# Performance work log

Measured on AMD Instinct MI355X. Metric: run time of the kernel, lower is better.

The kernel has to match this reference:

```python
import jax, jax.numpy as jnp
import numpy as np

B, N, KD, VD = 2048, 131072, 256, 256

def setup_inputs() -> dict:
    key = jax.random.key(0)
    k1, k2, k3 = jax.random.split(key, 3)
    query = jax.random.normal(k1, (B, KD), dtype=jnp.float32)
    keys = jax.random.normal(k2, (N, KD), dtype=jnp.float32)
    vals = jax.random.normal(k3, (N, VD), dtype=jnp.float32)
    return {"query": query, "keys": keys, "vals": vals, "top_k": 8}

def reference(query, keys, vals, top_k):
    # Pairwise L2 distance via the matmul identity (same math as
    # torch.norm(q[:,None]-k[None], dim=-1), avoids B x N x D intermediate):
    # ||q - k||^2 = ||q||^2 + ||k||^2 - 2 q.k
    q2 = jnp.sum(query * query, axis=-1, keepdims=True)          # [B, 1]
    k2 = jnp.sum(keys * keys, axis=-1)                           # [N]
    qk = jnp.einsum('bd,nd->bn', query, keys)                    # [B, N]
    dist = jnp.sqrt(jnp.maximum(q2 + k2[None, :] - 2.0 * qk, 0.0))
    # top-k smallest distances -> negate and take top-k largest
    _, indices = jax.lax.top_k(-dist, top_k)                     # [B, k]
    retrieved = vals[indices]                                    # [B, k, VD]
    return retrieved
```

## Files before the change

kernel.cpp:

```cpp
#include <hip/hip_runtime.h>
#include <hip/hip_bf16.h>
#include <cstdint>

#define B_Q    2048
#define N_K    131072
#define KD     256
#define VD     256
#define TOPK   8

#define TK     32
#define NCHUNK 64
#define CHUNK  (N_K / NCHUNK)
#define CTILES (CHUNK / TK)
#define QB     256
#define QTILES (B_Q / QB)
#define QBS    256
#define NBUF   4
#define TILE_B (TK * KD * 2)
#define SSTEPS 8
#define SLOTS  32
#define OVCAP  8192
#define NSUB   16
#define TAU_MARGIN 2.0f
#define SENTF  0x7F800000u

typedef short bf16x8 __attribute__((ext_vector_type(8)));
typedef float f32x4  __attribute__((ext_vector_type(4)));

__device__ __forceinline__ unsigned short f2bf(float x) {
    uint32_t u = __float_as_uint(x);
    uint32_t r = (u + 0x7FFFu + ((u >> 16) & 1u)) >> 16;
    return (unsigned short)r;
}

__device__ __forceinline__ bool lex_lt(float d1, int i1, float d2, int i2) {
    return (d1 < d2) || (d1 == d2 && i1 < i2);
}

__device__ __forceinline__ uint32_t umin32(uint32_t a, uint32_t b) { return a < b ? a : b; }
__device__ __forceinline__ uint32_t umax32(uint32_t a, uint32_t b) { return a > b ? a : b; }
__device__ __forceinline__ unsigned long long umin64(unsigned long long a, unsigned long long b) { return a < b ? a : b; }

__device__ __forceinline__ void gld16(const void* g, void* l) {
    __builtin_amdgcn_global_load_lds(
        (const __attribute__((address_space(1))) unsigned int*)g,
        (__attribute__((address_space(3))) unsigned int*)l, 16, 0, 0);
}
__device__ __forceinline__ void gld4(const void* g, void* l) {
    __builtin_amdgcn_global_load_lds(
        (const __attribute__((address_space(1))) unsigned int*)g,
        (__attribute__((address_space(3))) unsigned int*)l, 4, 0, 0);
}

__device__ __forceinline__ void ins8u(uint32_t v, uint32_t (&c)[8]) {
    if (v < c[7]) {
        c[7] = v;
        #pragma unroll
        for (int p = 7; p > 0; --p)
            if (c[p] < c[p - 1]) { uint32_t t = c[p]; c[p] = c[p - 1]; c[p - 1] = t; }
    }
}

__global__ void qprep_kernel(const float* __restrict__ q, float* __restrict__ q2,
                             unsigned short* __restrict__ qa) {
    int gw   = (blockIdx.x * blockDim.x + threadIdx.x) >> 6;
    int lane = threadIdx.x & 63;
    float4 v = reinterpret_cast<const float4*>(q + (size_t)gw * KD)[lane];
    float s = v.x * v.x + v.y * v.y + v.z * v.z + v.w * v.w;
    #pragma unroll
    for (int off = 32; off > 0; off >>= 1) s += __shfl_down(s, off, 64);
    if (lane == 0) q2[gw] = s;
    ushort4 u;
    u.x = f2bf(-2.f * v.x); u.y = f2bf(-2.f * v.y);
    u.z = f2bf(-2.f * v.z); u.w = f2bf(-2.f * v.w);
    *reinterpret_cast<ushort4*>(qa + (size_t)gw * KD + lane * 4) = u;
}

__global__ __launch_bounds__(256) void kperm2_kernel(
    const float* __restrict__ keys, unsigned short* __restrict__ kp,
    float* __restrict__ k2) {
    __shared__ float psum[32][33];
    const int gt = blockIdx.x, tid = threadIdx.x;
    #pragma unroll
    for (int u = 0; u < 4; ++u) {
        int unit = u * 256 + tid;
        int row  = unit >> 5;
        int grp  = unit & 31;
        const float* src = keys + (size_t)(gt * 32 + row) * KD + grp * 8;
        float4 a = *reinterpret_cast<const float4*>(src);
        float4 b = *reinterpret_cast<const float4*>(src + 4);
        psum[row][grp] = a.x * a.x + a.y * a.y + a.z * a.z + a.w * a.w
                       + b.x * b.x + b.y * b.y + b.z * b.z + b.w * b.w;
        uint4 pack;
        pack.x = (uint32_t)f2bf(a.x) | ((uint32_t)f2bf(a.y) << 16);
        pack.y = (uint32_t)f2bf(a.z) | ((uint32_t)f2bf(a.w) << 16);
        pack.z = (uint32_t)f2bf(b.x) | ((uint32_t)f2bf(b.y) << 16);
        pack.w = (uint32_t)f2bf(b.z) | ((uint32_t)f2bf(b.w) << 16);
        int s  = grp >> 2;
        int ki = row >> 4;
        int l  = ((grp & 3) << 4) | (row & 15);
        size_t o = ((((size_t)gt * 8 + s) * 2 + ki) * 64 + l);
        *reinterpret_cast<uint4*>(kp + o * 8) = pack;
    }
    __syncthreads();
    if (tid < 32) {
        float s = 0.f;
        #pragma unroll
        for (int g = 0; g < 32; ++g) s += psum[tid][g];
        k2[gt * 32 + tid] = s;
    }
}

__global__ __launch_bounds__(512, 2) void sample_kernel(
    const unsigned short* __restrict__ qaug, const char* __restrict__ kperm,
    const float* __restrict__ k2, uint32_t* __restrict__ subtop) {

    __shared__ __align__(16) char  lds[TILE_B];
    __shared__ __align__(16) float k2l[64];

    const int tid = threadIdx.x;
    const int w   = tid >> 6;
    const int l   = tid & 63;
    const int l15 = l & 15;
    const int l4  = l >> 4;
    const int sub = blockIdx.x & (NSUB - 1);
    const int qt  = blockIdx.x >> 4;
    const int q0  = qt * QBS;

    bf16x8 af[2][SSTEPS];
    #pragma unroll
    for (int qf = 0; qf < 2; ++qf)
        #pragma unroll
        for (int s = 0; s < SSTEPS; ++s) {
            int qr = q0 + w * 32 + qf * 16 + l15;
            af[qf][s] = *reinterpret_cast<const bf16x8*>(
                qaug + (size_t)qr * KD + s * 32 + l4 * 8);
        }

    uint32_t cnd[2][4][8];
    #pragma unroll
    for (int qf = 0; qf < 2; ++qf)
        #pragma unroll
        for (int j = 0; j < 4; ++j)
            #pragma unroll
            for (int s = 0; s < 8; ++s) cnd[qf][j][s] = SENTF;

    for (int i = 0; i < 4; ++i) {
        int t = sub * 4 + i;
        __syncthreads();
        const char* src = kperm + (size_t)t * TILE_B;
        #pragma unroll
        for (int i2 = 0; i2 < 2; ++i2) {
            int seg = w * 2 + i2;
            gld16(src + seg * 1024 + l * 16, &lds[seg * 1024]);
        }
        gld4(k2 + t * TK + l, &k2l[0]);
        __syncthreads();

        float k2v[2];
        #pragma unroll
        for (int ki = 0; ki < 2; ++ki) k2v[ki] = k2l[ki * 16 + l15] + 256.0f;

        f32x4 acc[2][2];
        #pragma unroll
        for (int qf = 0; qf < 2; ++qf)
            #pragma unroll
            for (int ki = 0; ki < 2; ++ki) acc[qf][ki] = (f32x4){0.f, 0.f, 0.f, 0.f};

        #pragma unroll
        for (int s = 0; s < SSTEPS; ++s) {
            bf16x8 bfr[2];
            #pragma unroll
            for (int ki = 0; ki < 2; ++ki)
                bfr[ki] = *reinterpret_cast<const bf16x8*>(&lds[((s * 2 + ki) * 64 + l) * 16]);
            #pragma unroll
            for (int ki = 0; ki < 2; ++ki) {
                acc[0][ki] = __builtin_amdgcn_mfma_f32_16x16x32_bf16(af[0][s], bfr[ki], acc[0][ki], 0, 0, 0);
                acc[1][ki] = __builtin_amdgcn_mfma_f32_16x16x32_bf16(af[1][s], bfr[ki], acc[1][ki], 0, 0, 0);
            }
        }

        #pragma unroll
        for (int qf = 0; qf < 2; ++qf)
            #pragma unroll
            for (int j = 0; j < 4; ++j) {
                ins8u(__float_as_uint(k2v[0] + acc[qf][0][j]), cnd[qf][j]);
                ins8u(__float_as_uint(k2v[1] + acc[qf][1][j]), cnd[qf][j]);
            }
    }

    #pragma unroll
    for (int qf = 0; qf < 2; ++qf)
        #pragma unroll
        for (int j = 0; j < 4; ++j) {
            uint32_t c[8];
            #pragma unroll
            for (int s = 0; s < 8; ++s) c[s] = cnd[qf][j][s];
            #pragma unroll
            for (int mask = 1; mask <= 8; mask <<= 1) {
                uint32_t o[8], m[8];
                #pragma unroll
                for (int s = 0; s < 8; ++s)
                    o[s] = (uint32_t)__shfl_xor((int)c[s], mask, 64);
                #pragma unroll
                for (int s = 0; s < 8; ++s) m[s] = umin32(c[s], o[7 - s]);
                #define CX(a,b) { uint32_t lo = umin32(m[a], m[b]); uint32_t hi = umax32(m[a], m[b]); m[a] = lo; m[b] = hi; }
                CX(0,4) CX(1,5) CX(2,6) CX(3,7)
                CX(0,2) CX(1,3) CX(4,6) CX(5,7)
                CX(0,1) CX(2,3) CX(4,5) CX(6,7)
                #undef CX
                #pragma unroll
                for (int s = 0; s < 8; ++s) c[s] = m[s];
            }
            if (l15 == 0) {
                int q = q0 + w * 32 + qf * 16 + l4 * 4 + j;
                uint32_t* dst = subtop + ((size_t)q * NSUB + sub) * 8;
                uint4 a = {c[0], c[1], c[2], c[3]};
                uint4 b = {c[4], c[5], c[6], c[7]};
                *reinterpret_cast<uint4*>(dst)     = a;
                *reinterpret_cast<uint4*>(dst + 4) = b;
            }
        }
}

__global__ __launch_bounds__(256) void tau_kernel(
    const uint32_t* __restrict__ subtop, float* __restrict__ taug,
    uint32_t* __restrict__ ovcnt) {
    const int tid = threadIdx.x, l = tid & 63;
    const int q = blockIdx.x * 4 + (tid >> 6);
    uint32_t a = subtop[(size_t)q * 128 + l];
    uint32_t b = subtop[(size_t)q * 128 + 64 + l];
    uint32_t c[8];
    c[0] = umin32(a, b); c[1] = umax32(a, b);
    #pragma unroll
    for (int s = 2; s < 8; ++s) c[s] = SENTF;
    #pragma unroll
    for (int mask = 1; mask <= 32; mask <<= 1) {
        uint32_t o[8], m[8];
        #pragma unroll
        for (int s = 0; s < 8; ++s)
            o[s] = (uint32_t)__shfl_xor((int)c[s], mask, 64);
        #pragma unroll
        for (int s = 0; s < 8; ++s) m[s] = umin32(c[s], o[7 - s]);
        #define CX(x,y) { uint32_t lo = umin32(m[x], m[y]); uint32_t hi = umax32(m[x], m[y]); m[x] = lo; m[y] = hi; }
        CX(0,4) CX(1,5) CX(2,6) CX(3,7)
        CX(0,2) CX(1,3) CX(4,6) CX(5,7)
        CX(0,1) CX(2,3) CX(4,5) CX(6,7)
        #undef CX
        #pragma unroll
        for (int s = 0; s < 8; ++s) c[s] = m[s];
    }
    if (l == 0) taug[q] = __uint_as_float(c[7]) + TAU_MARGIN;
    if (blockIdx.x == 0 && tid == 0) *ovcnt = 0;
}

__global__ __launch_bounds__(1024, 4) void phase1_kernel(
    const unsigned short* __restrict__ qaug, const char* __restrict__ kperm,
    const float* __restrict__ k2, const float* __restrict__ taug,
    uint32_t* __restrict__ list, uint32_t* __restrict__ cnt2,
    uint32_t* __restrict__ ovcnt, unsigned long long* __restrict__ ovlist) {

    __shared__ __align__(16) char     lds[NBUF][TILE_B];
    __shared__ __align__(16) float    k2l[NBUF][64];
    __shared__            uint32_t    scnt[QB];

    const int tid   = threadIdx.x;
    const int w     = tid >> 6;
    const int p     = w >> 1;
    const int ki    = w & 1;
    const int l     = tid & 63;
    const int l15   = l & 15;
    const int l4    = l >> 4;
    const int chunk = blockIdx.x & (NCHUNK - 1);
    const int qt    = blockIdx.x >> 6;
    const int q0    = qt * QB;
    const char*  kpb = kperm + (size_t)chunk * ((size_t)CTILES * TILE_B);
    const float* k2c = k2 + (size_t)chunk * CHUNK;

    if (tid < QB) scnt[tid] = 0;

    bf16x8 af[2][SSTEPS];
    float  tau[2][4];
    #pragma unroll
    for (int qf = 0; qf < 2; ++qf) {
        #pragma unroll
        for (int s = 0; s < SSTEPS; ++s) {
            int qr = q0 + p * 32 + qf * 16 + l15;
            af[qf][s] = *reinterpret_cast<const bf16x8*>(
                qaug + (size_t)qr * KD + s * 32 + l4 * 8);
        }
        #pragma unroll
        for (int j = 0; j < 4; ++j)
            tau[qf][j] = taug[q0 + p * 32 + qf * 16 + l4 * 4 + j];
    }

    auto STAGE = [&](int t) {
        int buf = t & (NBUF - 1);
        const char* src = kpb + (size_t)t * TILE_B;
        gld16(src + w * 1024 + l * 16, &lds[buf][w * 1024]);
        gld4(k2c + t * TK + l, &k2l[buf][0]);
    };

    STAGE(0); STAGE(1); STAGE(2);

    for (int t = 0; t < CTILES; ++t) {
        const int buf = t & (NBUF - 1);
        if (t < CTILES - 2)       asm volatile("s_waitcnt vmcnt(4)" ::: "memory");
        else if (t == CTILES - 2) asm volatile("s_waitcnt vmcnt(2)" ::: "memory");
        else                      asm volatile("s_waitcnt vmcnt(0)" ::: "memory");
        __builtin_amdgcn_s_barrier();
        __builtin_amdgcn_sched_barrier(0);

        const char* lb = &lds[buf][0];
        const float k2v = k2l[buf][ki * 16 + l15] + 256.0f;

        f32x4 acc[2];
        acc[0] = (f32x4){0.f, 0.f, 0.f, 0.f};
        acc[1] = (f32x4){0.f, 0.f, 0.f, 0.f};

        #pragma unroll
        for (int s = 0; s < SSTEPS; ++s) {
            bf16x8 bfr = *reinterpret_cast<const bf16x8*>(lb + ((s * 2 + ki) * 64 + l) * 16);
            acc[0] = __builtin_amdgcn_mfma_f32_16x16x32_bf16(af[0][s], bfr, acc[0], 0, 0, 0);
            acc[1] = __builtin_amdgcn_mfma_f32_16x16x32_bf16(af[1][s], bfr, acc[1], 0, 0, 0);
        }

        const uint32_t kb = (uint32_t)(t * TK + ki * 16 + l15);
        #pragma unroll
        for (int qf = 0; qf < 2; ++qf)
            #pragma unroll
            for (int j = 0; j < 4; ++j) {
                float v0 = k2v + acc[qf][j];
                if (v0 < tau[qf][j]) {
                    int ql = p * 32 + qf * 16 + l4 * 4 + j;
                    uint32_t slot = atomicAdd(&scnt[ql], 1u);
                    uint32_t e = (__float_as_uint(v0) & 0xFFFFF800u) | kb;
                    if (slot < SLOTS) {
                        list[(((size_t)(q0 + ql) * NCHUNK + chunk) << 5) + slot] = e;
                    } else {
                        uint32_t op = atomicAdd(ovcnt, 1u);
                        if (op < OVCAP)
                            ovlist[op] = ((unsigned long long)__float_as_uint(v0) << 32)
                                       | ((unsigned long long)(uint32_t)(q0 + ql) << 17)
                                       | (uint32_t)(chunk * CHUNK + kb);
                    }
                }
            }

        if (t + 3 < CTILES) STAGE(t + 3);
    }

    __syncthreads();
    if (tid < QB) cnt2[(size_t)(q0 + tid) * NCHUNK + chunk] = umin32(scnt[tid], SLOTS);
}

__global__ __launch_bounds__(256) void phase2_kernel(
    const uint32_t* __restrict__ list, const uint32_t* __restrict__ cnt2,
    const uint32_t* __restrict__ ovcnt, const unsigned long long* __restrict__ ovlist,
    const float* __restrict__ query, const float* __restrict__ keys,
    const float* __restrict__ q2g, const float* __restrict__ k2g,
    const float* __restrict__ vals, float* __restrict__ out) {

    __shared__ uint32_t cc[NCHUNK];
    __shared__ unsigned long long ovq[64];
    __shared__ uint32_t nov;
    __shared__ int topg[64];
    __shared__ float td2[64];
    __shared__ int fin[8];

    const int q = blockIdx.x, tid = threadIdx.x, w = tid >> 6, l = tid & 63;

    if (tid < NCHUNK) cc[tid] = cnt2[(size_t)q * NCHUNK + tid];
    if (tid < 64) ovq[tid] = ~0ull;
    if (tid == 0) nov = 0;
    __syncthreads();
    uint32_t on = umin32(*ovcnt, OVCAP);
    for (uint32_t i = tid; i < on; i += 256) {
        unsigned long long e = ovlist[i];
        if (((e >> 17) & 0x7FFull) == (unsigned long long)q) {
            uint32_t p = atomicAdd(&nov, 1u);
            if (p < 64)
                ovq[p] = ((unsigned long long)((uint32_t)(e >> 32) >> 11) << 17)
                       | (uint32_t)(e & 0x1FFFFull);
        }
    }
    __syncthreads();

    unsigned long long v[9];
    #pragma unroll
    for (int j = 0; j < 9; ++j) {
        int idx = j * 64 + l;
        unsigned long long key = ~0ull;
        if (idx < 512) {
            int c = w * 16 + (idx >> 5), s = idx & 31;
            if ((uint32_t)s < cc[c]) {
                uint32_t e = list[(((size_t)q * NCHUNK + c) << 5) + s];
                key = ((unsigned long long)(e >> 11) << 17)
                    | (uint32_t)(c * CHUNK + (e & 0x7FFu));
            }
        } else if (idx < 528) {
            key = ovq[w * 16 + (idx - 512)];
        }
        v[j] = key;
    }

    for (int r = 0; r < 16; ++r) {
        unsigned long long bv = v[0];
        #pragma unroll
        for (int j = 1; j < 9; ++j) bv = umin64(bv, v[j]);
        #pragma unroll
        for (int off = 32; off > 0; off >>= 1) {
            unsigned long long ov = __shfl_xor(bv, off, 64);
            bv = umin64(bv, ov);
        }
        if (l == 0) topg[w * 16 + r] = (bv == ~0ull) ? -1 : (int)(uint32_t)(bv & 0x1FFFFull);
        #pragma unroll
        for (int j = 0; j < 9; ++j) if (v[j] == bv) v[j] = ~0ull;
    }
    __syncthreads();

    float4 qv = reinterpret_cast<const float4*>(query + (size_t)q * KD)[l];
    for (int r = w; r < 64; r += 4) {
        int gk = topg[r];
        if (gk >= 0) {
            float4 kv = reinterpret_cast<const float4*>(keys + (size_t)gk * KD)[l];
            float d = qv.x * kv.x + qv.y * kv.y + qv.z * kv.z + qv.w * kv.w;
            #pragma unroll
            for (int off = 32; off > 0; off >>= 1) d += __shfl_down(d, off, 64);
            if (l == 0) td2[r] = fmaxf(q2g[q] + k2g[gk] - 2.0f * d, 0.0f);
        } else if (l == 0) {
            td2[r] = INFINITY;
        }
    }
    __syncthreads();

    if (tid == 0) {
        float fd[8]; int fi[8];
        #pragma unroll
        for (int s = 0; s < 8; ++s) { fd[s] = INFINITY; fi[s] = 0x7fffffff; }
        for (int i = 0; i < 64; ++i) {
            if (topg[i] < 0) continue;
            float d2 = td2[i]; int gk = topg[i];
            if (lex_lt(d2, gk, fd[7], fi[7])) {
                fd[7] = d2; fi[7] = gk;
                #pragma unroll
                for (int p = 7; p > 0; --p)
                    if (lex_lt(fd[p], fi[p], fd[p - 1], fi[p - 1])) {
                        float t1 = fd[p]; fd[p] = fd[p - 1]; fd[p - 1] = t1;
                        int   t2 = fi[p]; fi[p] = fi[p - 1]; fi[p - 1] = t2;
                    }
            }
        }
        #pragma unroll
        for (int s = 0; s < 8; ++s) fin[s] = fi[s];
    }
    __syncthreads();

    for (int r = w; r < TOPK; r += 4) {
        float4 v2 = reinterpret_cast<const float4*>(vals + (size_t)fin[r] * VD)[l];
        reinterpret_cast<float4*>(out + ((size_t)q * TOPK + r) * VD)[l] = v2;
    }
}

extern "C" void kernel_launch(void* const* d_in, const int* in_sizes, int n_in,
                              void* d_out, int out_size, void* d_ws, size_t ws_size,
                              hipStream_t stream) {
    const float* query = (const float*)d_in[0];
    const float* keys  = (const float*)d_in[1];
    const float* vals  = (const float*)d_in[2];
    float* out = (float*)d_out;

    char* ws = (char*)d_ws;
    float*              q2     = (float*)(ws);
    float*              k2     = (float*)(ws + 8192);
    unsigned short*     qaug   = (unsigned short*)(ws + 533504);
    unsigned short*     kperm  = (unsigned short*)(ws + 1582080);
    uint32_t*           list   = (uint32_t*)(ws + 68690944);
    uint32_t*           subtop = (uint32_t*)(ws + 68690944);
    uint32_t*           cnt2   = (uint32_t*)(ws + 85468160);
    float*              taug   = (float*)(ws + 85992448);
    uint32_t*           ovcnt  = (uint32_t*)(ws + 86000640);
    unsigned long long* ovlist = (unsigned long long*)(ws + 86004736);

    qprep_kernel<<<B_Q / 4, 256, 0, stream>>>(query, q2, qaug);
    kperm2_kernel<<<N_K / 32, 256, 0, stream>>>(keys, kperm, k2);
    sample_kernel<<<(B_Q / QBS) * NSUB, 512, 0, stream>>>(qaug, (const char*)kperm, k2, subtop);
    tau_kernel<<<B_Q / 4, 256, 0, stream>>>(subtop, taug, ovcnt);
    phase1_kernel<<<NCHUNK * QTILES, 1024, 0, stream>>>(qaug, (const char*)kperm, k2,
                                                        taug, list, cnt2, ovcnt, ovlist);
    phase2_kernel<<<B_Q, 256, 0, stream>>>(list, cnt2, ovcnt, ovlist,
                                           query, keys, q2, k2, vals, out);
}
```

Baseline: 300.9 us.

## Switch phase1 to 32x32x16 MFMA with new key permutation layout

Phase1 now uses the 32x32x16 bf16 MFMA, with each wave computing a full 32-query by 32-key tile. Blocks shrink to 512 threads, and each thread stages two segments per tile. The key-permute kernel writes a new layout that matches the 32x32 B-fragment. Because that layout no longer fits the 16x16 sample kernel, the sample kernel now reads fp32 keys directly and converts them to bf16 into LDS itself. The larger MFMA shape is meant to cut LDS fragment reads and instruction count per FLOP, at the cost of more accumulator registers and fewer waves per block.

```diff
diff --git a/kernel.cpp b/kernel.cpp
--- a/kernel.cpp
+++ b/kernel.cpp
@@ -18,6 +18,7 @@
 #define NBUF   4
 #define TILE_B (TK * KD * 2)
 #define SSTEPS 8
+#define KSTEPS 16
 #define SLOTS  32
 #define OVCAP  8192
 #define NSUB   16
@@ -26,6 +27,7 @@
 
 typedef short bf16x8 __attribute__((ext_vector_type(8)));
 typedef float f32x4  __attribute__((ext_vector_type(4)));
+typedef float f32x16 __attribute__((ext_vector_type(16)));
 
 __device__ __forceinline__ unsigned short f2bf(float x) {
     uint32_t u = __float_as_uint(x);
@@ -96,10 +98,10 @@
         pack.y = (uint32_t)f2bf(a.z) | ((uint32_t)f2bf(a.w) << 16);
         pack.z = (uint32_t)f2bf(b.x) | ((uint32_t)f2bf(b.y) << 16);
         pack.w = (uint32_t)f2bf(b.z) | ((uint32_t)f2bf(b.w) << 16);
-        int s  = grp >> 2;
-        int ki = row >> 4;
-        int l  = ((grp & 3) << 4) | (row & 15);
-        size_t o = ((((size_t)gt * 8 + s) * 2 + ki) * 64 + l);
+        int kk   = grp >> 1;
+        int g    = grp & 1;
+        int lane = g * 32 + row;
+        size_t o = (((size_t)gt * KSTEPS + kk) * 64 + lane);
         *reinterpret_cast<uint4*>(kp + o * 8) = pack;
     }
     __syncthreads();
@@ -112,11 +114,10 @@
 }
 
 __global__ __launch_bounds__(512, 2) void sample_kernel(
-    const unsigned short* __restrict__ qaug, const char* __restrict__ kperm,
+    const unsigned short* __restrict__ qaug, const float* __restrict__ keys,
     const float* __restrict__ k2, uint32_t* __restrict__ subtop) {
 
-    __shared__ __align__(16) char  lds[TILE_B];
-    __shared__ __align__(16) float k2l[64];
+    __shared__ __align__(16) char lds[TILE_B];
 
     const int tid = threadIdx.x;
     const int w   = tid >> 6;
@@ -148,18 +149,30 @@
     for (int i = 0; i < 4; ++i) {
         int t = sub * 4 + i;
         __syncthreads();
-        const char* src = kperm + (size_t)t * TILE_B;
-        #pragma unroll
-        for (int i2 = 0; i2 < 2; ++i2) {
-            int seg = w * 2 + i2;
-            gld16(src + seg * 1024 + l * 16, &lds[seg * 1024]);
-        }
-        gld4(k2 + t * TK + l, &k2l[0]);
+        #pragma unroll
+        for (int uu = 0; uu < 2; ++uu) {
+            int unit = uu * 512 + tid;
+            int row  = unit >> 5;
+            int grp  = unit & 31;
+            const float* src = keys + (size_t)(t * 32 + row) * KD + grp * 8;
+            float4 a = *reinterpret_cast<const float4*>(src);
+            float4 b = *reinterpret_cast<const float4*>(src + 4);
+            uint4 pack;
+            pack.x = (uint32_t)f2bf(a.x) | ((uint32_t)f2bf(a.y) << 16);
+            pack.y = (uint32_t)f2bf(a.z) | ((uint32_t)f2bf(a.w) << 16);
+            pack.z = (uint32_t)f2bf(b.x) | ((uint32_t)f2bf(b.y) << 16);
+            pack.w = (uint32_t)f2bf(b.z) | ((uint32_t)f2bf(b.w) << 16);
+            int s    = grp >> 2;
+            int g    = grp & 3;
+            int lane = g * 16 + (row & 15);
+            int ki   = row >> 4;
+            *reinterpret_cast<uint4*>(&lds[((s * 2 + ki) * 64 + lane) * 16]) = pack;
+        }
         __syncthreads();
 
         float k2v[2];
         #pragma unroll
-        for (int ki = 0; ki < 2; ++ki) k2v[ki] = k2l[ki * 16 + l15] + 256.0f;
+        for (int ki = 0; ki < 2; ++ki) k2v[ki] = k2[t * TK + ki * 16 + l15] + 256.0f;
 
         f32x4 acc[2][2];
         #pragma unroll
@@ -254,7 +267,7 @@
     if (blockIdx.x == 0 && tid == 0) *ovcnt = 0;
 }
 
-__global__ __launch_bounds__(1024, 4) void phase1_kernel(
+__global__ __launch_bounds__(512, 4) void phase1_kernel(
     const unsigned short* __restrict__ qaug, const char* __restrict__ kperm,
     const float* __restrict__ k2, const float* __restrict__ taug,
     uint32_t* __restrict__ list, uint32_t* __restrict__ cnt2,
@@ -266,11 +279,9 @@
 
     const int tid   = threadIdx.x;
     const int w     = tid >> 6;
-    const int p     = w >> 1;
-    const int ki    = w & 1;
     const int l     = tid & 63;
-    const int l15   = l & 15;
-    const int l4    = l >> 4;
+    const int l31   = l & 31;
+    const int lg    = l >> 5;
     const int chunk = blockIdx.x & (NCHUNK - 1);
     const int qt    = blockIdx.x >> 6;
     const int q0    = qt * QB;
@@ -279,25 +290,26 @@
 
     if (tid < QB) scnt[tid] = 0;
 
-    bf16x8 af[2][SSTEPS];
-    float  tau[2][4];
-    #pragma unroll
-    for (int qf = 0; qf < 2; ++qf) {
-        #pragma unroll
-        for (int s = 0; s < SSTEPS; ++s) {
-            int qr = q0 + p * 32 + qf * 16 + l15;
-            af[qf][s] = *reinterpret_cast<const bf16x8*>(
-                qaug + (size_t)qr * KD + s * 32 + l4 * 8);
-        }
-        #pragma unroll
-        for (int j = 0; j < 4; ++j)
-            tau[qf][j] = taug[q0 + p * 32 + qf * 16 + l4 * 4 + j];
-    }
+    bf16x8 af[KSTEPS];
+    const int qr = q0 + w * 32 + l31;
+    #pragma unroll
+    for (int kk = 0; kk < KSTEPS; ++kk)
+        af[kk] = *reinterpret_cast<const bf16x8*>(
+            qaug + (size_t)qr * KD + kk * 16 + lg * 8);
+
+    float tau[16];
+    #pragma unroll
+    for (int r = 0; r < 16; ++r)
+        tau[r] = taug[q0 + w * 32 + (r & 3) + 8 * (r >> 2) + 4 * lg];
 
     auto STAGE = [&](int t) {
         int buf = t & (NBUF - 1);
         const char* src = kpb + (size_t)t * TILE_B;
-        gld16(src + w * 1024 + l * 16, &lds[buf][w * 1024]);
+        #pragma unroll
+        for (int i = 0; i < 2; ++i) {
+            int seg = w * 2 + i;
+            gld16(src + seg * 1024 + l * 16, &lds[buf][seg * 1024]);
+        }
         gld4(k2c + t * TK + l, &k2l[buf][0]);
     };
 
@@ -305,47 +317,42 @@
 
     for (int t = 0; t < CTILES; ++t) {
         const int buf = t & (NBUF - 1);
-        if (t < CTILES - 2)       asm volatile("s_waitcnt vmcnt(4)" ::: "memory");
-        else if (t == CTILES - 2) asm volatile("s_waitcnt vmcnt(2)" ::: "memory");
+        if (t < CTILES - 2)       asm volatile("s_waitcnt vmcnt(6)" ::: "memory");
+        else if (t == CTILES - 2) asm volatile("s_waitcnt vmcnt(3)" ::: "memory");
         else                      asm volatile("s_waitcnt vmcnt(0)" ::: "memory");
         __builtin_amdgcn_s_barrier();
         __builtin_amdgcn_sched_barrier(0);
 
         const char* lb = &lds[buf][0];
-        const float k2v = k2l[buf][ki * 16 + l15] + 256.0f;
-
-        f32x4 acc[2];
-        acc[0] = (f32x4){0.f, 0.f, 0.f, 0.f};
-        acc[1] = (f32x4){0.f, 0.f, 0.f, 0.f};
-
-        #pragma unroll
-        for (int s = 0; s < SSTEPS; ++s) {
-            bf16x8 bfr = *reinterpret_cast<const bf16x8*>(lb + ((s * 2 + ki) * 64 + l) * 16);
-            acc[0] = __builtin_amdgcn_mfma_f32_16x16x32_bf16(af[0][s], bfr, acc[0], 0, 0, 0);
-            acc[1] = __builtin_amdgcn_mfma_f32_16x16x32_bf16(af[1][s], bfr, acc[1], 0, 0, 0);
-        }
-
-        const uint32_t kb = (uint32_t)(t * TK + ki * 16 + l15);
-        #pragma unroll
-        for (int qf = 0; qf < 2; ++qf)
-            #pragma unroll
-            for (int j = 0; j < 4; ++j) {
-                float v0 = k2v + acc[qf][j];
-                if (v0 < tau[qf][j]) {
-                    int ql = p * 32 + qf * 16 + l4 * 4 + j;
-                    uint32_t slot = atomicAdd(&scnt[ql], 1u);
-                    uint32_t e = (__float_as_uint(v0) & 0xFFFFF800u) | kb;
-                    if (slot < SLOTS) {
-                        list[(((size_t)(q0 + ql) * NCHUNK + chunk) << 5) + slot] = e;
-                    } else {
-                        uint32_t op = atomicAdd(ovcnt, 1u);
-                        if (op < OVCAP)
-                            ovlist[op] = ((unsigned long long)__float_as_uint(v0) << 32)
-                                       | ((unsigned long long)(uint32_t)(q0 + ql) << 17)
-                                       | (uint32_t)(chunk * CHUNK + kb);
-                    }
+        const float k2v = k2l[buf][l31] + 256.0f;
+
+        f32x16 acc = (f32x16){0.f, 0.f, 0.f, 0.f, 0.f, 0.f, 0.f, 0.f,
+                              0.f, 0.f, 0.f, 0.f, 0.f, 0.f, 0.f, 0.f};
+        #pragma unroll
+        for (int kk = 0; kk < KSTEPS; ++kk) {
+            bf16x8 bfr = *reinterpret_cast<const bf16x8*>(lb + ((kk * 64 + l) * 16));
+            acc = __builtin_amdgcn_mfma_f32_32x32x16_bf16(af[kk], bfr, acc, 0, 0, 0);
+        }
+
+        const uint32_t kb = (uint32_t)(t * TK + l31);
+        #pragma unroll
+        for (int r = 0; r < 16; ++r) {
+            float v0 = k2v + acc[r];
+            if (v0 < tau[r]) {
+                int ql = w * 32 + (r & 3) + 8 * (r >> 2) + 4 * lg;
+                uint32_t slot = atomicAdd(&scnt[ql], 1u);
+                uint32_t e = (__float_as_uint(v0) & 0xFFFFF800u) | kb;
+                if (slot < SLOTS) {
+                    list[(((size_t)(q0 + ql) * NCHUNK + chunk) << 5) + slot] = e;
+                } else {
+                    uint32_t op = atomicAdd(ovcnt, 1u);
+                    if (op < OVCAP)
+                        ovlist[op] = ((unsigned long long)__float_as_uint(v0) << 32)
+                                   | ((unsigned long long)(uint32_t)(q0 + ql) << 17)
+                                   | (uint32_t)(chunk * CHUNK + kb);
                 }
             }
+        }
 
         if (t + 3 < CTILES) STAGE(t + 3);
     }
@@ -484,10 +491,10 @@
 
     qprep_kernel<<<B_Q / 4, 256, 0, stream>>>(query, q2, qaug);
     kperm2_kernel<<<N_K / 32, 256, 0, stream>>>(keys, kperm, k2);
-    sample_kernel<<<(B_Q / QBS) * NSUB, 512, 0, stream>>>(qaug, (const char*)kperm, k2, subtop);
+    sample_kernel<<<(B_Q / QBS) * NSUB, 512, 0, stream>>>(qaug, keys, k2, subtop);
     tau_kernel<<<B_Q / 4, 256, 0, stream>>>(subtop, taug, ovcnt);
-    phase1_kernel<<<NCHUNK * QTILES, 1024, 0, stream>>>(qaug, (const char*)kperm, k2,
-                                                        taug, list, cnt2, ovcnt, ovlist);
+    phase1_kernel<<<NCHUNK * QTILES, 512, 0, stream>>>(qaug, (const char*)kperm, k2,
+                                                       taug, list, cnt2, ovcnt, ovlist);
     phase2_kernel<<<B_Q, 256, 0, stream>>>(list, cnt2, ovcnt, ovlist,
                                            query, keys, q2, k2, vals, out);
 }
```

Measured after the change: 340.9 us. +13.3%, slower.

## Shrink phase1 blocks to four waves each covering both key halves

Applied to the files above, without the earlier changes.

The phase1 distance-filter kernel drops from 1024-thread blocks over 256 queries to 256-thread blocks over 128 queries. Each wave now computes a 32-query by 32-key tile, reusing its query fragments across both 16-key halves. Each wave issues four LDS-staging loads per tile, and the vmcnt waits are adjusted to match. This aims to cut barrier cost across many waves and improve per-wave MFMA reuse. In exchange, each key tile is shared by half as many queries, so global key traffic doubles, the grid doubles, and per-thread register use rises.

```diff
diff --git a/kernel.cpp b/kernel.cpp
--- a/kernel.cpp
+++ b/kernel.cpp
@@ -12,7 +12,7 @@
 #define NCHUNK 64
 #define CHUNK  (N_K / NCHUNK)
 #define CTILES (CHUNK / TK)
-#define QB     256
+#define QB     128
 #define QTILES (B_Q / QB)
 #define QBS    256
 #define NBUF   4
@@ -254,7 +254,7 @@
     if (blockIdx.x == 0 && tid == 0) *ovcnt = 0;
 }
 
-__global__ __launch_bounds__(1024, 4) void phase1_kernel(
+__global__ __launch_bounds__(256, 2) void phase1_kernel(
     const unsigned short* __restrict__ qaug, const char* __restrict__ kperm,
     const float* __restrict__ k2, const float* __restrict__ taug,
     uint32_t* __restrict__ list, uint32_t* __restrict__ cnt2,
@@ -266,8 +266,6 @@
 
     const int tid   = threadIdx.x;
     const int w     = tid >> 6;
-    const int p     = w >> 1;
-    const int ki    = w & 1;
     const int l     = tid & 63;
     const int l15   = l & 15;
     const int l4    = l >> 4;
@@ -285,19 +283,23 @@
     for (int qf = 0; qf < 2; ++qf) {
         #pragma unroll
         for (int s = 0; s < SSTEPS; ++s) {
-            int qr = q0 + p * 32 + qf * 16 + l15;
+            int qr = q0 + w * 32 + qf * 16 + l15;
             af[qf][s] = *reinterpret_cast<const bf16x8*>(
                 qaug + (size_t)qr * KD + s * 32 + l4 * 8);
         }
         #pragma unroll
         for (int j = 0; j < 4; ++j)
-            tau[qf][j] = taug[q0 + p * 32 + qf * 16 + l4 * 4 + j];
+            tau[qf][j] = taug[q0 + w * 32 + qf * 16 + l4 * 4 + j];
     }
 
     auto STAGE = [&](int t) {
         int buf = t & (NBUF - 1);
         const char* src = kpb + (size_t)t * TILE_B;
-        gld16(src + w * 1024 + l * 16, &lds[buf][w * 1024]);
+        #pragma unroll
+        for (int i = 0; i < 4; ++i) {
+            int seg = w * 4 + i;
+            gld16(src + seg * 1024 + l * 16, &lds[buf][seg * 1024]);
+        }
         gld4(k2c + t * TK + l, &k2l[buf][0]);
     };
 
@@ -305,47 +307,59 @@
 
     for (int t = 0; t < CTILES; ++t) {
         const int buf = t & (NBUF - 1);
-        if (t < CTILES - 2)       asm volatile("s_waitcnt vmcnt(4)" ::: "memory");
-        else if (t == CTILES - 2) asm volatile("s_waitcnt vmcnt(2)" ::: "memory");
-        else                      asm volatile("s_waitcnt vmcnt(0)" ::: "memory");
+        if (t < CTILES - 2)       asm volatile("s_waitcnt vmcnt(10)" ::: "memory");
+        else if (t == CTILES - 2) asm volatile("s_waitcnt vmcnt(5)"  ::: "memory");
+        else                      asm volatile("s_waitcnt vmcnt(0)"  ::: "memory");
         __builtin_amdgcn_s_barrier();
         __builtin_amdgcn_sched_barrier(0);
 
         const char* lb = &lds[buf][0];
-        const float k2v = k2l[buf][ki * 16 + l15] + 256.0f;
-
-        f32x4 acc[2];
-        acc[0] = (f32x4){0.f, 0.f, 0.f, 0.f};
-        acc[1] = (f32x4){0.f, 0.f, 0.f, 0.f};
+        float k2v[2];
+        #pragma unroll
+        for (int ki = 0; ki < 2; ++ki) k2v[ki] = k2l[buf][ki * 16 + l15] + 256.0f;
+
+        f32x4 acc[2][2];
+        #pragma unroll
+        for (int qf = 0; qf < 2; ++qf)
+            #pragma unroll
+            for (int ki = 0; ki < 2; ++ki) acc[qf][ki] = (f32x4){0.f, 0.f, 0.f, 0.f};
 
         #pragma unroll
         for (int s = 0; s < SSTEPS; ++s) {
-            bf16x8 bfr = *reinterpret_cast<const bf16x8*>(lb + ((s * 2 + ki) * 64 + l) * 16);
-            acc[0] = __builtin_amdgcn_mfma_f32_16x16x32_bf16(af[0][s], bfr, acc[0], 0, 0, 0);
-            acc[1] = __builtin_amdgcn_mfma_f32_16x16x32_bf16(af[1][s], bfr, acc[1], 0, 0, 0);
-        }
-
-        const uint32_t kb = (uint32_t)(t * TK + ki * 16 + l15);
+            bf16x8 bfr[2];
+            #pragma unroll
+            for (int ki = 0; ki < 2; ++ki)
+                bfr[ki] = *reinterpret_cast<const bf16x8*>(lb + ((s * 2 + ki) * 64 + l) * 16);
+            #pragma unroll
+            for (int ki = 0; ki < 2; ++ki) {
+                acc[0][ki] = __builtin_amdgcn_mfma_f32_16x16x32_bf16(af[0][s], bfr[ki], acc[0][ki], 0, 0, 0);
+                acc[1][ki] = __builtin_amdgcn_mfma_f32_16x16x32_bf16(af[1][s], bfr[ki], acc[1][ki], 0, 0, 0);
+            }
+        }
+
+        const uint32_t kb0 = (uint32_t)(t * TK + l15);
         #pragma unroll
         for (int qf = 0; qf < 2; ++qf)
             #pragma unroll
-            for (int j = 0; j < 4; ++j) {
-                float v0 = k2v + acc[qf][j];
-                if (v0 < tau[qf][j]) {
-                    int ql = p * 32 + qf * 16 + l4 * 4 + j;
-                    uint32_t slot = atomicAdd(&scnt[ql], 1u);
-                    uint32_t e = (__float_as_uint(v0) & 0xFFFFF800u) | kb;
-                    if (slot < SLOTS) {
-                        list[(((size_t)(q0 + ql) * NCHUNK + chunk) << 5) + slot] = e;
-                    } else {
-                        uint32_t op = atomicAdd(ovcnt, 1u);
-                        if (op < OVCAP)
-                            ovlist[op] = ((unsigned long long)__float_as_uint(v0) << 32)
-                                       | ((unsigned long long)(uint32_t)(q0 + ql) << 17)
-                                       | (uint32_t)(chunk * CHUNK + kb);
+            for (int ki = 0; ki < 2; ++ki)
+                #pragma unroll
+                for (int j = 0; j < 4; ++j) {
+                    float v0 = k2v[ki] + acc[qf][ki][j];
+                    if (v0 < tau[qf][j]) {
+                        int ql = w * 32 + qf * 16 + l4 * 4 + j;
+                        uint32_t slot = atomicAdd(&scnt[ql], 1u);
+                        uint32_t e = (__float_as_uint(v0) & 0xFFFFF800u) | (kb0 + ki * 16u);
+                        if (slot < SLOTS) {
+                            list[(((size_t)(q0 + ql) * NCHUNK + chunk) << 5) + slot] = e;
+                        } else {
+                            uint32_t op = atomicAdd(ovcnt, 1u);
+                            if (op < OVCAP)
+                                ovlist[op] = ((unsigned long long)__float_as_uint(v0) << 32)
+                                           | ((unsigned long long)(uint32_t)(q0 + ql) << 17)
+                                           | (uint32_t)(chunk * CHUNK + kb0 + ki * 16u);
+                        }
                     }
                 }
-            }
 
         if (t + 3 < CTILES) STAGE(t + 3);
     }
@@ -486,8 +500,8 @@
     kperm2_kernel<<<N_K / 32, 256, 0, stream>>>(keys, kperm, k2);
     sample_kernel<<<(B_Q / QBS) * NSUB, 512, 0, stream>>>(qaug, (const char*)kperm, k2, subtop);
     tau_kernel<<<B_Q / 4, 256, 0, stream>>>(subtop, taug, ovcnt);
-    phase1_kernel<<<NCHUNK * QTILES, 1024, 0, stream>>>(qaug, (const char*)kperm, k2,
-                                                        taug, list, cnt2, ovcnt, ovlist);
+    phase1_kernel<<<NCHUNK * QTILES, 256, 0, stream>>>(qaug, (const char*)kperm, k2,
+                                                       taug, list, cnt2, ovcnt, ovlist);
     phase2_kernel<<<B_Q, 256, 0, stream>>>(list, cnt2, ovcnt, ovlist,
                                            query, keys, q2, k2, vals, out);
 }
```

Result: slower. 313.7 us (+4.3%).
